# Optimization experiments

Hardware: AMD Instinct MI355X
Metric: run time of the kernel (lower is better)

The kernel has to match this reference:

```python
import jax, jax.numpy as jnp
import numpy as np

HIDDEN = 2048
HEADS = 32
HEAD_DIM = HIDDEN // HEADS  # 64
MAX_POS = 512
TABLE = 2 * MAX_POS - 1  # 1023


def setup_inputs() -> dict:
    key = jax.random.key(0)
    k = jax.random.split(key, 6)
    B, S = 16, 512
    return {
        "hidden_states": jax.random.normal(k[0], (B, S, HIDDEN), dtype=jnp.float32),
        "wq": jax.random.normal(k[1], (HIDDEN, HIDDEN), dtype=jnp.float32) * 0.02,
        "wk": jax.random.normal(k[2], (HIDDEN, HIDDEN), dtype=jnp.float32) * 0.02,
        "wv": jax.random.normal(k[3], (HIDDEN, HIDDEN), dtype=jnp.float32) * 0.02,
        "wo": jax.random.normal(k[4], (HIDDEN, HIDDEN), dtype=jnp.float32) * 0.02,
        "rel_pos": jax.random.normal(k[5], (TABLE, HEAD_DIM), dtype=jnp.float32),
    }


def _rel_bias(rel_pos, seq_len):
    pos = jnp.arange(seq_len)
    rel = pos[None, :] - pos[:, None] + (MAX_POS - 1)  # [S, S]
    rel = jnp.clip(rel, 0, TABLE - 1)
    return rel_pos[rel].mean(axis=-1)  # [S, S]


def reference(hidden_states, wq, wk, wv, wo, rel_pos):
    B, S, _ = hidden_states.shape
    scale = jnp.sqrt(jnp.float32(HEAD_DIM))
    # nn.Linear(x) = x @ W.T
    q = (hidden_states @ wq.T).reshape(B, S, HEADS, HEAD_DIM).transpose(0, 2, 1, 3)
    k = (hidden_states @ wk.T).reshape(B, S, HEADS, HEAD_DIM).transpose(0, 2, 1, 3)
    v = (hidden_states @ wv.T).reshape(B, S, HEADS, HEAD_DIM).transpose(0, 2, 1, 3)
    scores = jnp.einsum("bhqd,bhkd->bhqk", q, k) / scale
    scores = scores + _rel_bias(rel_pos, S)[None, None]  # seq_len <= 512 path
    attn = jax.nn.softmax(scores, axis=-1)
    ctx = jnp.einsum("bhqk,bhkd->bhqd", attn, v)
    ctx = ctx.transpose(0, 2, 1, 3).reshape(B, S, HIDDEN)
    return ctx @ wo.T
```

## Files before the change

### kernel.cpp

```cpp
#include <hip/hip_runtime.h>

typedef __attribute__((ext_vector_type(8))) short bf16x8;
typedef __attribute__((ext_vector_type(4))) float f32x4;
typedef const __attribute__((address_space(3))) unsigned short* lds_cp;

#define DEVI __device__ __forceinline__

template <int N> struct IC { static constexpr int v = N; };

DEVI unsigned short f2bf(float f) {
  union { float f; unsigned u; } v; v.f = f;
  unsigned r = v.u + 0x7FFFu + ((v.u >> 16) & 1u);
  return (unsigned short)(r >> 16);
}

DEVI void gload16(const void* g, void* l) {
  __builtin_amdgcn_global_load_lds(
      (const __attribute__((address_space(1))) unsigned int*)g,
      (__attribute__((address_space(3))) unsigned int*)l, 16, 0, 0);
}

template <int OFF>
DEVI bf16x8 lreadT(lds_cp p) {
  bf16x8 r;
  asm volatile("ds_read_b128 %0, %1 offset:%2" : "=v"(r) : "v"(p), "i"(OFF));
  return r;
}

template <int OFF>
DEVI void read_af(lds_cp a0, lds_cp a1, bf16x8 (&f)[4][2]) {
  f[0][0] = lreadT<OFF + 0>(a0);    f[0][1] = lreadT<OFF + 0>(a1);
  f[1][0] = lreadT<OFF + 2048>(a0); f[1][1] = lreadT<OFF + 2048>(a1);
  f[2][0] = lreadT<OFF + 4096>(a0); f[2][1] = lreadT<OFF + 4096>(a1);
  f[3][0] = lreadT<OFF + 6144>(a0); f[3][1] = lreadT<OFF + 6144>(a1);
}
template <int OFF>
DEVI void read_bq(lds_cp b0, lds_cp b1, bf16x8 (&f)[2][2]) {
  f[0][0] = lreadT<OFF + 0>(b0);    f[0][1] = lreadT<OFF + 0>(b1);
  f[1][0] = lreadT<OFF + 2048>(b0); f[1][1] = lreadT<OFF + 2048>(b1);
}

#define MFMA16(a, b, c) __builtin_amdgcn_mfma_f32_16x16x32_bf16(a, b, c, 0, 0, 0)
#define LGKM(n) asm volatile("s_waitcnt lgkmcnt(" #n ")")
#define SBAR() __builtin_amdgcn_sched_barrier(0)

__global__ void cvt_kernel(const float* __restrict__ in,
                           unsigned short* __restrict__ out, int n4) {
  int i = blockIdx.x * blockDim.x + threadIdx.x;
  if (i < n4) {
    float4 v = ((const float4*)in)[i];
    ushort4 o;
    o.x = f2bf(v.x); o.y = f2bf(v.y); o.z = f2bf(v.z); o.w = f2bf(v.w);
    ((ushort4*)out)[i] = o;
  }
}

__global__ void cvt4_kernel(const float* __restrict__ a,
                            const float* __restrict__ b,
                            const float* __restrict__ c,
                            const float* __restrict__ d,
                            unsigned short* __restrict__ out) {
  int i = blockIdx.x * blockDim.x + threadIdx.x;
  const int w = i >> 20, l = i & 1048575;
  const float* s = (w == 0) ? a : (w == 1) ? b : (w == 2) ? c : d;
  float4 v = ((const float4*)s)[l];
  ushort4 o;
  o.x = f2bf(v.x); o.y = f2bf(v.y); o.z = f2bf(v.z); o.w = f2bf(v.w);
  ((ushort4*)out)[i] = o;
}

__global__ void bias_kernel(const float* __restrict__ rel_pos,
                            float* __restrict__ bias1d) {
  int t = blockIdx.x * blockDim.x + threadIdx.x;
  if (t < 1023) {
    const float* r = rel_pos + t * 64;
    float s = 0.f;
#pragma unroll
    for (int d = 0; d < 64; ++d) s += r[d];
    bias1d[t] = s * (1.44269504f / 64.0f);
  }
}

template <int MODE, int NT>
__global__ __launch_bounds__(512, 2) void gemm256(
    const unsigned short* __restrict__ A, const unsigned short* __restrict__ B,
    void* __restrict__ Cout, void* __restrict__ Cout2, void* __restrict__ Cout3) {
  __shared__ unsigned short As[2][16384];
  __shared__ unsigned short Bs[2][16384];

  const int tid = threadIdx.x;
  const int logical = (blockIdx.x & 7) * (4 * NT) + (blockIdx.x >> 3);
  const int nt = logical % NT, mt = logical / NT;
  const int m0 = mt * 256, n0 = nt * 256;
  const int lane = tid & 63, wid = tid >> 6;
  const int wr = wid >> 2, wc = wid & 3;
  const int g = lane >> 4, c = lane & 15;

  const int srow = tid >> 3, sj = (tid & 7) ^ (srow & 7);
  const unsigned short* pA0[2];
  const unsigned short* pB0[2];
  unsigned short* lA0[2];
  unsigned short* lB0[2];
#pragma unroll
  for (int ch = 0; ch < 2; ++ch) {
    const int row = ch * 64 + srow;
    pA0[ch] = A + (size_t)(m0 + row) * 2048u + sj * 8;
    pB0[ch] = B + (size_t)(n0 + row) * 2048u + sj * 8;
    const int slot = ch * 512 + tid;
    lA0[ch] = &As[0][slot * 8];
    lB0[ch] = &Bs[0][slot * 8];
  }

  const int rA = wr * 128 + c;
  const int rB = wc * 64 + c;
  lds_cp aA0 = (lds_cp)&As[0][rA * 64 + (((0 + g) ^ (rA & 7)) * 8)];
  lds_cp aA1 = (lds_cp)&As[0][rA * 64 + (((4 + g) ^ (rA & 7)) * 8)];
  lds_cp aB0 = (lds_cp)&Bs[0][rB * 64 + (((0 + g) ^ (rB & 7)) * 8)];
  lds_cp aB1 = (lds_cp)&Bs[0][rB * 64 + (((4 + g) ^ (rB & 7)) * 8)];

  f32x4 acc[8][4];
#pragma unroll
  for (int i = 0; i < 8; ++i)
#pragma unroll
    for (int j = 0; j < 4; ++j) acc[i][j] = (f32x4){0.f, 0.f, 0.f, 0.f};

  bf16x8 afl[4][2], afh[4][2], bq0[2][2], bq1[2][2];

#pragma unroll
  for (int ch = 0; ch < 2; ++ch) {
    gload16(pA0[ch], lA0[ch]);
    gload16(pA0[ch] + 262144, lA0[ch] + 8192);
    gload16(pB0[ch], lB0[ch]);
    gload16(pB0[ch] + 262144, lB0[ch] + 8192);
  }
#pragma unroll
  for (int ch = 0; ch < 2; ++ch) {
    gload16(pA0[ch] + 64, lA0[ch] + 16384);
    gload16(pA0[ch] + 262144 + 64, lA0[ch] + 8192 + 16384);
    gload16(pB0[ch] + 64, lB0[ch] + 16384);
    gload16(pB0[ch] + 262144 + 64, lB0[ch] + 8192 + 16384);
  }
  asm volatile("s_waitcnt vmcnt(8)" ::: "memory");
  SBAR();
  __builtin_amdgcn_s_barrier();
  read_af<0>(aA0, aA1, afl);
  read_bq<0>(aB0, aB1, bq0);

  auto ktile = [&](auto B_, auto NB_, auto S_, auto LD_, int kt) {
    constexpr int BOFF = decltype(B_)::v;
    constexpr int NBOFF = decltype(NB_)::v;
    constexpr int S = decltype(S_)::v;
    constexpr int LD = decltype(LD_)::v;

    read_bq<BOFF + 4096>(aB0, aB1, bq1);
    read_af<BOFF + 8192>(aA0, aA1, afh);

    LGKM(12);
    SBAR();
    __builtin_amdgcn_s_setprio(1);
#pragma unroll
    for (int kk = 0; kk < 2; ++kk)
#pragma unroll
      for (int mi = 0; mi < 4; ++mi)
#pragma unroll
        for (int ni = 0; ni < 2; ++ni)
          acc[mi][ni] = MFMA16(afl[mi][kk], bq0[ni][kk], acc[mi][ni]);
    __builtin_amdgcn_s_setprio(0);

    LGKM(8);
    SBAR();
    __builtin_amdgcn_s_setprio(1);
#pragma unroll
    for (int kk = 0; kk < 2; ++kk)
#pragma unroll
      for (int mi = 0; mi < 4; ++mi)
#pragma unroll
        for (int ni = 0; ni < 2; ++ni)
          acc[mi][ni + 2] = MFMA16(afl[mi][kk], bq1[ni][kk], acc[mi][ni + 2]);
    __builtin_amdgcn_s_setprio(0);

    LGKM(0);
    SBAR();
    __builtin_amdgcn_s_barrier();
    if (kt + 2 < 32) {
      gload16(pB0[0] + S, lB0[0] + LD);
      gload16(pB0[1] + S, lB0[1] + LD);
      gload16(pB0[0] + 262144 + S, lB0[0] + 8192 + LD);
      gload16(pB0[1] + 262144 + S, lB0[1] + 8192 + LD);
      gload16(pA0[0] + S, lA0[0] + LD);
      gload16(pA0[1] + S, lA0[1] + LD);
      gload16(pA0[0] + 262144 + S, lA0[0] + 8192 + LD);
      gload16(pA0[1] + 262144 + S, lA0[1] + 8192 + LD);
    }

    __builtin_amdgcn_s_setprio(1);
#pragma unroll
    for (int kk = 0; kk < 2; ++kk)
#pragma unroll
      for (int mi = 0; mi < 4; ++mi)
#pragma unroll
        for (int ni = 0; ni < 2; ++ni)
          acc[mi + 4][ni] = MFMA16(afh[mi][kk], bq0[ni][kk], acc[mi + 4][ni]);
    __builtin_amdgcn_s_setprio(0);

    if (kt < 30) {
      asm volatile("s_waitcnt vmcnt(8)" ::: "memory");
    } else {
      asm volatile("s_waitcnt vmcnt(0)" ::: "memory");
    }
    SBAR();
    __builtin_amdgcn_s_barrier();
    if (kt + 1 < 32) {
      read_af<NBOFF>(aA0, aA1, afl);
      read_bq<NBOFF>(aB0, aB1, bq0);
    }
    __builtin_amdgcn_s_setprio(1);
#pragma unroll
    for (int kk = 0; kk < 2; ++kk)
#pragma unroll
      for (int mi = 0; mi < 4; ++mi)
#pragma unroll
        for (int ni = 0; ni < 2; ++ni)
          acc[mi + 4][ni + 2] = MFMA16(afh[mi][kk], bq1[ni][kk], acc[mi + 4][ni + 2]);
    __builtin_amdgcn_s_setprio(0);
  };

  for (int t2 = 0; t2 < 16; ++t2) {
    ktile(IC<0>{}, IC<32768>{}, IC<128>{}, IC<0>{}, 2 * t2);
    ktile(IC<32768>{}, IC<0>{}, IC<192>{}, IC<16384>{}, 2 * t2 + 1);
#pragma unroll
    for (int ch = 0; ch < 2; ++ch) { pA0[ch] += 128; pB0[ch] += 128; }
  }

  const int rbase = m0 + wr * 128 + g * 4;
  const int cbase = n0 + wc * 64 + c;
  if (MODE == 0) {
    float* O = (float*)Cout;
#pragma unroll
    for (int mi = 0; mi < 8; ++mi)
#pragma unroll
      for (int ni = 0; ni < 4; ++ni)
#pragma unroll
        for (int rr = 0; rr < 4; ++rr)
          O[(size_t)(rbase + mi * 16 + rr) * 2048u + (cbase + ni * 16)] =
              acc[mi][ni][rr];
  } else {
    const int qsel = cbase >> 11;
    if (qsel < 2) {
      unsigned short* O = (unsigned short*)(qsel == 0 ? Cout : Cout2);
#pragma unroll
      for (int mi = 0; mi < 8; ++mi)
#pragma unroll
        for (int ni = 0; ni < 4; ++ni)
#pragma unroll
          for (int rr = 0; rr < 4; ++rr)
            O[(size_t)(rbase + mi * 16 + rr) * 2048u +
              ((cbase + ni * 16) & 2047)] = f2bf(acc[mi][ni][rr]);
    } else {
      unsigned short* O = (unsigned short*)Cout3;
#pragma unroll
      for (int mi = 0; mi < 8; ++mi)
#pragma unroll
        for (int ni = 0; ni < 4; ++ni) {
          const int row = rbase + mi * 16;
          const int col = (cbase + ni * 16) & 2047;
          const int bq_ = row >> 9, s = row & 511;
          const int hh = col >> 6, dd = col & 63;
          ushort4 o;
          o.x = f2bf(acc[mi][ni][0]);
          o.y = f2bf(acc[mi][ni][1]);
          o.z = f2bf(acc[mi][ni][2]);
          o.w = f2bf(acc[mi][ni][3]);
          *(ushort4*)(O + ((size_t)((bq_ * 32 + hh) * 64 + dd) << 9) + s) = o;
        }
    }
  }
}

__global__ __launch_bounds__(256, 3) void attn_kernel(
    const unsigned short* __restrict__ Q, const unsigned short* __restrict__ K,
    const unsigned short* __restrict__ VT, const float* __restrict__ bias1d,
    unsigned short* __restrict__ CTX) {
  __shared__ unsigned short Ksh[2][4096];
  __shared__ unsigned short Vsh[2][4096];
  __shared__ unsigned short Pb[4][2048];
  __shared__ float bl[1024];

  const int tid = threadIdx.x;
  const int wave = tid >> 6;
  const int lane = tid & 63;
  const int g = lane >> 4, c = lane & 15;

  const int logical = (blockIdx.x & 7) * 256 + (blockIdx.x >> 3);
  const int qc = logical & 3;
  const int bh = logical >> 2;
  const int b = bh >> 5, h = bh & 31;
  const int qrow0 = qc * 128 + wave * 32;

  for (int i = tid; i < 1023; i += 256) bl[i] = bias1d[i];

  bf16x8 aq[2][2];
  {
    const unsigned short* qb =
        Q + (size_t)(b * 512 + qrow0 + c) * 2048u + h * 64 + g * 8;
#pragma unroll
    for (int mi = 0; mi < 2; ++mi)
#pragma unroll
      for (int kk = 0; kk < 2; ++kk)
        aq[mi][kk] = *(const bf16x8*)(qb + mi * 16 * 2048 + kk * 32);
  }

  const unsigned short* kgb = K + (size_t)(b * 512) * 2048u + h * 64;
  const unsigned short* vgb = VT + (size_t)(bh * 64) * 512u;

  auto stage = [&](int buf, int kt) {
#pragma unroll
    for (int half = 0; half < 2; ++half) {
      const int slot = half * 256 + wave * 64 + lane;
      const int row = slot >> 3;
      const int j = (slot & 7) ^ (row & 7);
      gload16(kgb + (size_t)(kt * 64 + row) * 2048u + j * 8,
              &Ksh[buf][slot * 8]);
      gload16(vgb + (size_t)row * 512u + kt * 64 + j * 8, &Vsh[buf][slot * 8]);
    }
  };

  f32x4 o[2][4];
#pragma unroll
  for (int mi = 0; mi < 2; ++mi)
#pragma unroll
    for (int di = 0; di < 4; ++di) o[mi][di] = (f32x4){0.f, 0.f, 0.f, 0.f};
  float lreg[2][4];
#pragma unroll
  for (int mi = 0; mi < 2; ++mi)
#pragma unroll
    for (int rr = 0; rr < 4; ++rr) lreg[mi][rr] = 0.f;

  stage(0, 0);
  __syncthreads();

  const float SSCALE = 0.125f * 1.44269504f;

  for (int kt = 0; kt < 8; ++kt) {
    const int buf = kt & 1;
    if (kt < 7) stage(buf ^ 1, kt + 1);

    f32x4 s[2][4];
#pragma unroll
    for (int ni = 0; ni < 4; ++ni) {
      const unsigned short* kr = &Ksh[buf][(ni * 16 + c) * 64];
      bf16x8 bk0 = *(const bf16x8*)(kr + ((0 + g) ^ (c & 7)) * 8);
      bf16x8 bk1 = *(const bf16x8*)(kr + ((4 + g) ^ (c & 7)) * 8);
#pragma unroll
      for (int mi = 0; mi < 2; ++mi) {
        f32x4 z = (f32x4){0.f, 0.f, 0.f, 0.f};
        z = MFMA16(aq[mi][0], bk0, z);
        z = MFMA16(aq[mi][1], bk1, z);
        s[mi][ni] = z;
      }
    }

    unsigned short* pw = &Pb[wave][0];
#pragma unroll
    for (int mi = 0; mi < 2; ++mi)
#pragma unroll
      for (int rr = 0; rr < 4; ++rr) {
        const int prow = mi * 16 + g * 4 + rr;
        const int off0 = kt * 64 + c - (qrow0 + prow) + 511;
        float e0 = __builtin_amdgcn_exp2f(s[mi][0][rr] * SSCALE + bl[off0]);
        float e1 = __builtin_amdgcn_exp2f(s[mi][1][rr] * SSCALE + bl[off0 + 16]);
        float e2 = __builtin_amdgcn_exp2f(s[mi][2][rr] * SSCALE + bl[off0 + 32]);
        float e3 = __builtin_amdgcn_exp2f(s[mi][3][rr] * SSCALE + bl[off0 + 48]);
        lreg[mi][rr] += (e0 + e1) + (e2 + e3);
        const int rx = prow * 64, sw = (c >> 3) ^ (prow & 7), cl = c & 7;
        pw[rx + ((0 ^ sw) * 8 | cl)] = f2bf(e0);
        pw[rx + ((2 ^ sw) * 8 | cl)] = f2bf(e1);
        pw[rx + ((4 ^ sw) * 8 | cl)] = f2bf(e2);
        pw[rx + ((6 ^ sw) * 8 | cl)] = f2bf(e3);
      }

#pragma unroll
    for (int kk = 0; kk < 2; ++kk) {
      bf16x8 pa0 =
          *(const bf16x8*)(pw + (0 + c) * 64 + ((kk * 4 + g) ^ (c & 7)) * 8);
      bf16x8 pa1 =
          *(const bf16x8*)(pw + (16 + c) * 64 + ((kk * 4 + g) ^ (c & 7)) * 8);
#pragma unroll
      for (int di = 0; di < 4; ++di) {
        bf16x8 vb = *(const bf16x8*)(&Vsh[buf][(di * 16 + c) * 64 +
                                               ((kk * 4 + g) ^ (c & 7)) * 8]);
        o[0][di] = MFMA16(pa0, vb, o[0][di]);
        o[1][di] = MFMA16(pa1, vb, o[1][di]);
      }
    }
    __syncthreads();
  }

#pragma unroll
  for (int mi = 0; mi < 2; ++mi)
#pragma unroll
    for (int rr = 0; rr < 4; ++rr) {
      float l = lreg[mi][rr];
      l += __shfl_xor(l, 1);
      l += __shfl_xor(l, 2);
      l += __shfl_xor(l, 4);
      l += __shfl_xor(l, 8);
      const float rl = __builtin_amdgcn_rcpf(l);
      unsigned short* ob =
          CTX + (size_t)(b * 512 + qrow0 + mi * 16 + g * 4 + rr) * 2048u +
          h * 64 + c;
#pragma unroll
      for (int di = 0; di < 4; ++di) ob[di * 16] = f2bf(o[mi][di][rr] * rl);
    }
}

extern "C" void kernel_launch(void* const* d_in, const int* in_sizes, int n_in,
                              void* d_out, int out_size, void* d_ws,
                              size_t ws_size, hipStream_t stream) {
  const float* x = (const float*)d_in[0];
  const float* wq = (const float*)d_in[1];
  const float* wk = (const float*)d_in[2];
  const float* wv = (const float*)d_in[3];
  const float* wo = (const float*)d_in[4];
  const float* rel = (const float*)d_in[5];

  char* ws = (char*)d_ws;
  unsigned short* xb = (unsigned short*)(ws);
  unsigned short* wqb = (unsigned short*)(ws + 33554432);
  unsigned short* wob = wqb + 3 * 4194304;
  unsigned short* qb = (unsigned short*)(ws + 67108864);
  unsigned short* kb = qb + 16777216;
  unsigned short* vt = kb + 16777216;
  float* bias1 = (float*)(ws + 167772160);
  unsigned short* ctx = xb;

  cvt_kernel<<<16384, 256, 0, stream>>>(x, xb, 4194304);
  cvt4_kernel<<<16384, 256, 0, stream>>>(wq, wk, wv, wo, wqb);
  bias_kernel<<<4, 256, 0, stream>>>(rel, bias1);

  gemm256<3, 24><<<768, 512, 0, stream>>>(xb, wqb, qb, kb, vt);

  attn_kernel<<<2048, 256, 0, stream>>>(qb, kb, vt, bias1, ctx);

  gemm256<0, 8><<<256, 512, 0, stream>>>(ctx, wob, (float*)d_out, nullptr,
                                         nullptr);
}
```

Before: 385.0 us.

## Restructure GEMM k-loop into four barrier-separated phases with staggered loads

Reworks the main bf16 GEMM k-tile loop so each tile runs as four phases separated by workgroup barriers. A and B fragments are read from LDS just before use into a single A fragment buffer instead of double A buffers, cutting register pressure. B prefetch is now one tile ahead and interleaved with compute, while A prefetch stays two tiles ahead. This adds many extra s_barrier calls and removes the cross-tile LDS read overlap, which may stall the MFMA pipeline in exchange for fewer VGPRs and possibly better occupancy.

New measurement: 341.3 us. 1.13x faster.

```diff
diff --git a/kernel.cpp b/kernel.cpp
--- a/kernel.cpp
+++ b/kernel.cpp
@@ -124,7 +124,7 @@
 #pragma unroll
     for (int j = 0; j < 4; ++j) acc[i][j] = (f32x4){0.f, 0.f, 0.f, 0.f};
 
-  bf16x8 afl[4][2], afh[4][2], bq0[2][2], bq1[2][2];
+  bf16x8 af[4][2], bq0[2][2], bq1[2][2];
 
 #pragma unroll
   for (int ch = 0; ch < 2; ++ch) {
@@ -137,25 +137,27 @@
   for (int ch = 0; ch < 2; ++ch) {
     gload16(pA0[ch] + 64, lA0[ch] + 16384);
     gload16(pA0[ch] + 262144 + 64, lA0[ch] + 8192 + 16384);
-    gload16(pB0[ch] + 64, lB0[ch] + 16384);
-    gload16(pB0[ch] + 262144 + 64, lB0[ch] + 8192 + 16384);
-  }
-  asm volatile("s_waitcnt vmcnt(8)" ::: "memory");
+  }
+  asm volatile("s_waitcnt vmcnt(4)" ::: "memory");
   SBAR();
   __builtin_amdgcn_s_barrier();
-  read_af<0>(aA0, aA1, afl);
-  read_bq<0>(aB0, aB1, bq0);
-
-  auto ktile = [&](auto B_, auto NB_, auto S_, auto LD_, int kt) {
+
+  auto ktile = [&](auto B_, auto SB_, auto SA_, auto LB_, auto LA_, int kt) {
     constexpr int BOFF = decltype(B_)::v;
-    constexpr int NBOFF = decltype(NB_)::v;
-    constexpr int S = decltype(S_)::v;
-    constexpr int LD = decltype(LD_)::v;
-
-    read_bq<BOFF + 4096>(aB0, aB1, bq1);
-    read_af<BOFF + 8192>(aA0, aA1, afh);
-
-    LGKM(12);
+    constexpr int SB = decltype(SB_)::v;
+    constexpr int SA = decltype(SA_)::v;
+    constexpr int LB = decltype(LB_)::v;
+    constexpr int LA = decltype(LA_)::v;
+
+    read_af<BOFF>(aA0, aA1, af);
+    read_bq<BOFF>(aB0, aB1, bq0);
+    if (kt + 1 < 32) {
+      gload16(pB0[0] + SB, lB0[0] + LB);
+      gload16(pB0[1] + SB, lB0[1] + LB);
+    }
+    LGKM(8);
+    __builtin_amdgcn_s_barrier();
+    LGKM(0);
     SBAR();
     __builtin_amdgcn_s_setprio(1);
 #pragma unroll
@@ -164,10 +166,17 @@
       for (int mi = 0; mi < 4; ++mi)
 #pragma unroll
         for (int ni = 0; ni < 2; ++ni)
-          acc[mi][ni] = MFMA16(afl[mi][kk], bq0[ni][kk], acc[mi][ni]);
+          acc[mi][ni] = MFMA16(af[mi][kk], bq0[ni][kk], acc[mi][ni]);
     __builtin_amdgcn_s_setprio(0);
-
-    LGKM(8);
+    __builtin_amdgcn_s_barrier();
+
+    read_bq<BOFF + 4096>(aB0, aB1, bq1);
+    if (kt + 1 < 32) {
+      gload16(pB0[0] + 262144 + SB, lB0[0] + 8192 + LB);
+      gload16(pB0[1] + 262144 + SB, lB0[1] + 8192 + LB);
+    }
+    __builtin_amdgcn_s_barrier();
+    LGKM(0);
     SBAR();
     __builtin_amdgcn_s_setprio(1);
 #pragma unroll
@@ -176,44 +185,38 @@
       for (int mi = 0; mi < 4; ++mi)
 #pragma unroll
         for (int ni = 0; ni < 2; ++ni)
-          acc[mi][ni + 2] = MFMA16(afl[mi][kk], bq1[ni][kk], acc[mi][ni + 2]);
+          acc[mi][ni + 2] = MFMA16(af[mi][kk], bq1[ni][kk], acc[mi][ni + 2]);
     __builtin_amdgcn_s_setprio(0);
-
+    __builtin_amdgcn_s_barrier();
+
+    read_af<BOFF + 8192>(aA0, aA1, af);
+    __builtin_amdgcn_s_barrier();
     LGKM(0);
     SBAR();
-    __builtin_amdgcn_s_barrier();
+    __builtin_amdgcn_s_setprio(1);
+#pragma unroll
+    for (int kk = 0; kk < 2; ++kk)
+#pragma unroll
+      for (int mi = 0; mi < 4; ++mi)
+#pragma unroll
+        for (int ni = 0; ni < 2; ++ni)
+          acc[mi + 4][ni] = MFMA16(af[mi][kk], bq0[ni][kk], acc[mi + 4][ni]);
+    __builtin_amdgcn_s_setprio(0);
+    __builtin_amdgcn_s_barrier();
+
     if (kt + 2 < 32) {
-      gload16(pB0[0] + S, lB0[0] + LD);
-      gload16(pB0[1] + S, lB0[1] + LD);
-      gload16(pB0[0] + 262144 + S, lB0[0] + 8192 + LD);
-      gload16(pB0[1] + 262144 + S, lB0[1] + 8192 + LD);
-      gload16(pA0[0] + S, lA0[0] + LD);
-      gload16(pA0[1] + S, lA0[1] + LD);
-      gload16(pA0[0] + 262144 + S, lA0[0] + 8192 + LD);
-      gload16(pA0[1] + 262144 + S, lA0[1] + 8192 + LD);
-    }
-
-    __builtin_amdgcn_s_setprio(1);
-#pragma unroll
-    for (int kk = 0; kk < 2; ++kk)
-#pragma unroll
-      for (int mi = 0; mi < 4; ++mi)
-#pragma unroll
-        for (int ni = 0; ni < 2; ++ni)
-          acc[mi + 4][ni] = MFMA16(afh[mi][kk], bq0[ni][kk], acc[mi + 4][ni]);
-    __builtin_amdgcn_s_setprio(0);
-
+      gload16(pA0[0] + SA, lA0[0] + LA);
+      gload16(pA0[1] + SA, lA0[1] + LA);
+      gload16(pA0[0] + 262144 + SA, lA0[0] + 8192 + LA);
+      gload16(pA0[1] + 262144 + SA, lA0[1] + 8192 + LA);
+    }
     if (kt < 30) {
-      asm volatile("s_waitcnt vmcnt(8)" ::: "memory");
+      asm volatile("s_waitcnt vmcnt(4)" ::: "memory");
     } else {
       asm volatile("s_waitcnt vmcnt(0)" ::: "memory");
     }
     SBAR();
     __builtin_amdgcn_s_barrier();
-    if (kt + 1 < 32) {
-      read_af<NBOFF>(aA0, aA1, afl);
-      read_bq<NBOFF>(aB0, aB1, bq0);
-    }
     __builtin_amdgcn_s_setprio(1);
 #pragma unroll
     for (int kk = 0; kk < 2; ++kk)
@@ -221,13 +224,14 @@
       for (int mi = 0; mi < 4; ++mi)
 #pragma unroll
         for (int ni = 0; ni < 2; ++ni)
-          acc[mi + 4][ni + 2] = MFMA16(afh[mi][kk], bq1[ni][kk], acc[mi + 4][ni + 2]);
+          acc[mi + 4][ni + 2] = MFMA16(af[mi][kk], bq1[ni][kk], acc[mi + 4][ni + 2]);
     __builtin_amdgcn_s_setprio(0);
+    __builtin_amdgcn_s_barrier();
   };
 
   for (int t2 = 0; t2 < 16; ++t2) {
-    ktile(IC<0>{}, IC<32768>{}, IC<128>{}, IC<0>{}, 2 * t2);
-    ktile(IC<32768>{}, IC<0>{}, IC<192>{}, IC<16384>{}, 2 * t2 + 1);
+    ktile(IC<0>{}, IC<64>{}, IC<128>{}, IC<16384>{}, IC<0>{}, 2 * t2);
+    ktile(IC<32768>{}, IC<128>{}, IC<192>{}, IC<0>{}, IC<16384>{}, 2 * t2 + 1);
 #pragma unroll
     for (int ch = 0; ch < 2; ++ch) { pA0[ch] += 128; pB0[ch] += 128; }
   }
```
